# Kernel tuning notes

Measured on AMD Instinct MI355X. Metric: run time of the kernel, lower is better.

## Reference

```python
import jax, jax.numpy as jnp
import numpy as np

B, T, C, H = 4, 4096, 1024, 128

def setup_inputs() -> dict:
    key = jax.random.key(0)
    kx, kk, kq, kv = jax.random.split(key, 4)
    scale = 1.0 / np.sqrt(C)  # mimic Linear init scale
    return {
        'x':  jax.random.normal(kx, (B, T, C), dtype=jnp.float32),
        'Wk': jax.random.normal(kk, (C, H), dtype=jnp.float32) * scale,
        'Wq': jax.random.normal(kq, (C, H), dtype=jnp.float32) * scale,
        'Wv': jax.random.normal(kv, (C, H), dtype=jnp.float32) * scale,
    }

def reference(x, Wk, Wq, Wv):
    # x: [B,T,C]; projections to [B,T,H]
    k = jnp.einsum('btc,ch->bth', x, Wk)
    q = jnp.einsum('btc,ch->bth', x, Wq)
    v = jnp.einsum('btc,ch->bth', x, Wv)
    scale = jnp.asarray(x.shape[-1] and (k.shape[-1] ** -0.5), dtype=x.dtype)
    # scores: [B,T,T]
    scores = jnp.einsum('bqh,bkh->bqk', q, k) * scale
    Tn = x.shape[1]
    causal = jnp.tril(jnp.ones((Tn, Tn), dtype=bool))
    scores = jnp.where(causal[None, :, :], scores, -jnp.inf)
    attn = jax.nn.softmax(scores, axis=-1)
    # dropout=0.0 -> identity
    out = jnp.einsum('bqk,bkh->bqh', attn, v)
    return out
```

## Files before the change

kernel.cpp:

```cpp
#include <hip/hip_runtime.h>
#include <hip/hip_bf16.h>
#include <math.h>

#define B_ 4
#define T_ 4096
#define C_ 1024
#define H_ 128
#define SCALE 0.08838834764831845f
#define SCL2  0.12752934464f

typedef __attribute__((ext_vector_type(8))) short bf16x8;
typedef __attribute__((ext_vector_type(4))) float f32x4;

__device__ __forceinline__ unsigned short f2bf(float f) {
    union { float f; unsigned u; } x; x.f = f;
    unsigned r = x.u + 0x7FFF + ((x.u >> 16) & 1);
    return (unsigned short)(r >> 16);
}
__device__ __forceinline__ float bf2f(unsigned short u) {
    union { unsigned u; float f; } x; x.u = ((unsigned)u) << 16;
    return x.f;
}
__device__ __forceinline__ unsigned cvt_pk_bf16(float a, float b) {
    unsigned r;
    asm("v_cvt_pk_bf16_f32 %0, %1, %2" : "=v"(r) : "v"(a), "v"(b));
    return r;
}
__device__ __forceinline__ float vexp2(float x) {
    float r;
    asm("v_exp_f32 %0, %1" : "=v"(r) : "v"(x));
    return r;
}
__device__ __forceinline__ void cvt16(const float4& a, const float4& b,
                                      const float4& c, const float4& d,
                                      unsigned* t) {
    t[0]=cvt_pk_bf16(a.x,a.y); t[1]=cvt_pk_bf16(a.z,a.w);
    t[2]=cvt_pk_bf16(b.x,b.y); t[3]=cvt_pk_bf16(b.z,b.w);
    t[4]=cvt_pk_bf16(c.x,c.y); t[5]=cvt_pk_bf16(c.z,c.w);
    t[6]=cvt_pk_bf16(d.x,d.y); t[7]=cvt_pk_bf16(d.z,d.w);
}

#define GLOAD16(gsrc, ldst)                                                        \
    __builtin_amdgcn_global_load_lds(                                              \
        (const __attribute__((address_space(1))) unsigned int*)(gsrc),             \
        (__attribute__((address_space(3))) unsigned int*)(ldst), 16, 0, 0)

__global__ __launch_bounds__(256) void wtrans_kernel(
        const float* __restrict__ Wk, const float* __restrict__ Wq,
        const float* __restrict__ Wv, unsigned short* __restrict__ Wt) {
    int tid = blockIdx.x * 256 + threadIdx.x;
    int t = tid >> 17;
    int r = tid & 131071;
    int c = r >> 7;
    int h = r & 127;
    const float* W = (t == 0) ? Wk : (t == 1) ? Wq : Wv;
    Wt[t * 131072 + h * 1024 + c] = f2bf(W[r]);
}

__global__ __launch_bounds__(256, 2) void qkv_gemm6(
        const float* __restrict__ x, const unsigned short* __restrict__ Wt,
        unsigned short* __restrict__ qkv, unsigned short* __restrict__ vT) {
    __shared__ unsigned short As[2][64][72];
    __shared__ unsigned short Bs[2][192][64];

    const int n = blockIdx.x;
    const int mm = n & 255;
    const int nh = n >> 8;
    const int m0 = ((mm & 7) * 32 + (mm >> 3)) * 64;

    const int tid = threadIdx.x;
    const int lane = tid & 63;
    const int w = tid >> 6;
    const int fr = lane & 15;
    const int fq = lane >> 4;

    const int xrow = tid >> 2, xco = (tid & 3) * 16;
    const float* xsrc = x + (long)(m0 + xrow) * C_ + xco;
    const int brl = lane >> 3;
    const int bcolb = (((lane & 7) ^ brl) << 4);
    unsigned short* const bs_flat = &Bs[0][0][0];
    const unsigned short* wbase = Wt + (long)(nh * 192) * 1024;

    f32x4 acc[3][4];
#pragma unroll
    for (int i = 0; i < 3; i++)
#pragma unroll
        for (int rf = 0; rf < 4; rf++) acc[i][rf] = f32x4{0.f, 0.f, 0.f, 0.f};

    float4 xa0, xa1, xa2, xa3, xb0, xb1, xb2, xb3;
    xa0 = ((const float4*)xsrc)[0]; xa1 = ((const float4*)xsrc)[1];
    xa2 = ((const float4*)xsrc)[2]; xa3 = ((const float4*)xsrc)[3];
#pragma unroll
    for (int i = 0; i < 6; i++)
        GLOAD16(wbase + (long)(48*w + 8*i + brl) * 1024 + (bcolb >> 1),
                bs_flat + (w*6 + i) * 512);
    {
        unsigned tw[8];
        cvt16(xa0, xa1, xa2, xa3, tw);
        *(uint4*)&As[0][xrow][xco]     = uint4{tw[0], tw[1], tw[2], tw[3]};
        *(uint4*)&As[0][xrow][xco + 8] = uint4{tw[4], tw[5], tw[6], tw[7]};
    }
    {
        const float* xs = xsrc + 64;
        xa0 = ((const float4*)xs)[0]; xa1 = ((const float4*)xs)[1];
        xa2 = ((const float4*)xs)[2]; xa3 = ((const float4*)xs)[3];
    }

    int cur = 0;
    for (int k = 0; k < 16; ++k) {
        __syncthreads();
        const bool more  = (k + 1) < 16;
        const bool more2 = (k + 2) < 16;
        if (more) {
            if (more2) {
                const float* xs = xsrc + (k + 2) * 64;
                xb0 = ((const float4*)xs)[0]; xb1 = ((const float4*)xs)[1];
                xb2 = ((const float4*)xs)[2]; xb3 = ((const float4*)xs)[3];
            }
            const int boff = (cur ^ 1) * 12288;
#pragma unroll
            for (int i = 0; i < 6; i++)
                GLOAD16(wbase + (long)(48*w + 8*i + brl) * 1024 + (k + 1) * 64 + (bcolb >> 1),
                        bs_flat + boff + (w*6 + i) * 512);
            if (more2) asm volatile("s_waitcnt vmcnt(10)" ::: "memory");
            else       asm volatile("s_waitcnt vmcnt(6)" ::: "memory");
        } else {
            asm volatile("s_waitcnt vmcnt(0)" ::: "memory");
        }
        __syncthreads();

        const char* bsb = (const char*)bs_flat + cur * 24576;
        __builtin_amdgcn_s_setprio(1);
#pragma unroll
        for (int kk = 0; kk < 2; kk++) {
            bf16x8 a[4], bb[3];
#pragma unroll
            for (int rf = 0; rf < 4; rf++)
                a[rf] = *(const bf16x8*)&As[cur][rf*16 + fr][kk*32 + fq*8];
#pragma unroll
            for (int i = 0; i < 3; i++) {
                int row = (w*3 + i) * 16 + fr;
                bb[i] = *(const bf16x8*)(bsb + row*128 + ((((kk<<2) + fq) ^ (fr & 7)) << 4));
            }
#pragma unroll
            for (int i = 0; i < 3; i++)
#pragma unroll
                for (int rf = 0; rf < 4; rf++)
                    acc[i][rf] = __builtin_amdgcn_mfma_f32_16x16x32_bf16(
                        a[rf], bb[i], acc[i][rf], 0, 0, 0);
        }
        __builtin_amdgcn_s_setprio(0);

        if (more) {
            unsigned tw[8];
            cvt16(xa0, xa1, xa2, xa3, tw);
            *(uint4*)&As[cur ^ 1][xrow][xco]     = uint4{tw[0], tw[1], tw[2], tw[3]};
            *(uint4*)&As[cur ^ 1][xrow][xco + 8] = uint4{tw[4], tw[5], tw[6], tw[7]};
            xa0 = xb0; xa1 = xb1; xa2 = xb2; xa3 = xb3;
        }
        cur ^= 1;
    }

#pragma unroll
    for (int i = 0; i < 3; i++) {
        int nfg = nh*12 + w*3 + i;
        int t = nfg >> 3;
        int col = (nfg & 7) * 16 + fr;
        if (t < 2) {
#pragma unroll
            for (int rf = 0; rf < 4; rf++)
#pragma unroll
                for (int r = 0; r < 4; r++) {
                    int row = m0 + rf*16 + fq*4 + r;
                    qkv[(long)t * 2097152 + (long)row * 128 + col] = f2bf(acc[i][rf][r]);
                }
        } else {
            const int bb_ = m0 >> 12;
            const int trow = m0 & 4095;
#pragma unroll
            for (int rf = 0; rf < 4; rf++) {
                uint2 uu;
                uu.x = cvt_pk_bf16(acc[i][rf][0], acc[i][rf][1]);
                uu.y = cvt_pk_bf16(acc[i][rf][2], acc[i][rf][3]);
                *(uint2*)(vT + ((long)(bb_*128 + col)) * 4096 + trow + rf*16 + fq*4) = uu;
            }
        }
    }
}

__global__ __launch_bounds__(512, 4) void flash9_kernel(
        const unsigned short* __restrict__ qkv,
        const unsigned short* __restrict__ vT,
        unsigned short* __restrict__ po0, unsigned short* __restrict__ po1,
        unsigned short* __restrict__ po2, unsigned short* __restrict__ po3,
        float* __restrict__ pm, float* __restrict__ pl) {
    __shared__ unsigned short k_lds[2][64][128];
    __shared__ unsigned short v_lds[2][128][64];

    const int n = blockIdx.x;
    const int half = n >> 8;
    const int m = n & 255;
    const int b = (m & 7) >> 1;
    const int r = ((m >> 3) << 1) | (m & 1);
    const int jj = r & 31;
    const int pq = r >> 5;
    const int qt = half ? (31 - jj) : jj;
    const int p = half * 2 + pq;
    const int q0 = qt * 128;
    const int ntt = (qt + 1) * 2;
    const int t0 = (p * ntt) >> 2;
    const int t1 = ((p + 1) * ntt) >> 2;

    const int tid = threadIdx.x;
    const int w = tid >> 6;
    const int lane = tid & 63;
    const int fr = lane & 15;
    const int fq = lane >> 4;

    const unsigned short* kbase = qkv + (long)b * T_ * H_;
    const unsigned short* vbase = vT + (long)b * H_ * T_;

    const int kcolb0 = ((lane & 15) << 4) ^ ((((lane >> 4)) & 7) << 4);
    const int kcolb1 = ((lane & 15) << 4) ^ (((4 + (lane >> 4)) & 7) << 4);
    const int krl = lane >> 4;
    const int vrl = lane >> 3;
    const int vcolb = ((lane & 7) << 4) ^ (vrl << 4);
    unsigned short* const klds_flat = &k_lds[0][0][0];
    unsigned short* const vlds_flat = &v_lds[0][0][0];
    const int scol = ((fq ^ (fr & 7)) << 4);

    bf16x8 qf[4];
    {
        const unsigned short* qptr = qkv + 2097152 + ((long)b*T_ + q0 + w*16 + fr) * H_;
#pragma unroll
        for (int ks = 0; ks < 4; ks++)
            qf[ks] = *(const bf16x8*)(qptr + ks*32 + fq*8);
    }

    bf16x8 ones;
    {
        union { unsigned short s[8]; bf16x8 v; } oc;
#pragma unroll
        for (int i = 0; i < 8; i++) oc.s[i] = 0x3F80;
        ones = oc.v;
    }

    f32x4 acc[8];
#pragma unroll
    for (int i = 0; i < 8; i++) acc[i] = f32x4{0.f, 0.f, 0.f, 0.f};
    f32x4 acc_l = f32x4{0.f, 0.f, 0.f, 0.f};
    float m_r = -INFINITY;
    const int qrow = q0 + w*16 + fr;

    int cur = 0;
    if (t0 < t1) {
        const int kv0 = t0 * 64;
#pragma unroll
        for (int i = 0; i < 2; i++) {
            int kcolb = i ? kcolb1 : kcolb0;
            GLOAD16(kbase + (long)(kv0 + 8*w + 4*i + krl) * 128 + (kcolb >> 1),
                    klds_flat + w*1024 + i*512);
            GLOAD16(vbase + (long)(16*w + 8*i + vrl) * 4096 + kv0 + (vcolb >> 1),
                    vlds_flat + w*1024 + i*512);
        }
    }

    for (int t = t0; t < t1; ++t) {
        const int kv0 = t * 64;
        asm volatile("s_waitcnt vmcnt(0)" ::: "memory");
        __syncthreads();
        if (t + 1 < t1) {
            const int kv0n = kv0 + 64;
            const int boff = (cur ^ 1) * 8192;
#pragma unroll
            for (int i = 0; i < 2; i++) {
                int kcolb = i ? kcolb1 : kcolb0;
                GLOAD16(kbase + (long)(kv0n + 8*w + 4*i + krl) * 128 + (kcolb >> 1),
                        klds_flat + boff + w*1024 + i*512);
                GLOAD16(vbase + (long)(16*w + 8*i + vrl) * 4096 + kv0n + (vcolb >> 1),
                        vlds_flat + boff + w*1024 + i*512);
            }
        }

        const char* kl = (const char*)k_lds + cur*16384 + fr*256;
        const char* vl = (const char*)v_lds + cur*16384 + fr*128;

        f32x4 s[4];
#pragma unroll
        for (int sf = 0; sf < 4; sf++) s[sf] = f32x4{0.f,0.f,0.f,0.f};
        __builtin_amdgcn_s_setprio(1);
#pragma unroll
        for (int sf = 0; sf < 4; sf++)
#pragma unroll
            for (int ks = 0; ks < 4; ks++) {
                bf16x8 kf = *(const bf16x8*)(kl + sf*4096 + (scol ^ (ks << 6)));
                s[sf] = __builtin_amdgcn_mfma_f32_16x16x32_bf16(kf, qf[ks], s[sf], 0, 0, 0);
            }
        __builtin_amdgcn_s_setprio(0);

        float pmax = -INFINITY;
        if (kv0 + 63 > q0 + 16*w) {
#pragma unroll
            for (int sf = 0; sf < 4; sf++)
#pragma unroll
                for (int rr = 0; rr < 4; rr++) {
                    int kv = kv0 + sf*16 + fq*4 + rr;
                    float sv = s[sf][rr] * SCL2;
                    sv = (kv > qrow) ? -INFINITY : sv;
                    s[sf][rr] = sv;
                    pmax = fmaxf(pmax, sv);
                }
        } else {
#pragma unroll
            for (int sf = 0; sf < 4; sf++)
#pragma unroll
                for (int rr = 0; rr < 4; rr++) {
                    float sv = s[sf][rr] * SCL2;
                    s[sf][rr] = sv;
                    pmax = fmaxf(pmax, sv);
                }
        }

        const bool skip = __all((m_r > -1e37f) & (pmax - m_r <= 11.5f));
        float msub;
        if (skip) {
            msub = m_r;
        } else {
            float mx = fmaxf(pmax, __shfl_xor(pmax, 16, 64));
            mx = fmaxf(mx, __shfl_xor(mx, 32, 64));
            float mn = fmaxf(m_r, mx);
            msub = (mn == -INFINITY) ? 0.f : mn;
            float alpha = vexp2(m_r - msub);
            m_r = mn;
#pragma unroll
            for (int hf = 0; hf < 8; hf++)
#pragma unroll
                for (int rr = 0; rr < 4; rr++) acc[hf][rr] *= alpha;
#pragma unroll
            for (int rr = 0; rr < 4; rr++) acc_l[rr] *= alpha;
        }

        float pv[4][4];
#pragma unroll
        for (int sf = 0; sf < 4; sf++)
#pragma unroll
            for (int rr = 0; rr < 4; rr++)
                pv[sf][rr] = vexp2(s[sf][rr] - msub);

        unsigned pw[8];
#pragma unroll
        for (int sf = 0; sf < 4; sf++) {
            pw[2*sf]   = cvt_pk_bf16(pv[sf][0], pv[sf][1]);
            pw[2*sf+1] = cvt_pk_bf16(pv[sf][2], pv[sf][3]);
        }
        unsigned pbu[2][4];
        pbu[0][0]=0;pbu[0][1]=0;pbu[0][2]=0;pbu[0][3]=0;
        pbu[1][0]=0;pbu[1][1]=0;pbu[1][2]=0;pbu[1][3]=0;
        const int L1 = fr + 16 * ((fq & 1) * 2);
        const int L2 = L1 + 16;
        const int sel = (fq >> 1) & 1;
#pragma unroll
        for (int sf = 0; sf < 4; sf++) {
            unsigned w0 = (unsigned)__shfl((int)pw[2*sf],   L1, 64);
            unsigned w1 = (unsigned)__shfl((int)pw[2*sf+1], L1, 64);
            unsigned w2 = (unsigned)__shfl((int)pw[2*sf],   L2, 64);
            unsigned w3 = (unsigned)__shfl((int)pw[2*sf+1], L2, 64);
            if ((sf & 1) == sel) {
                int k2 = sf >> 1;
                pbu[k2][0] = w0; pbu[k2][1] = w1; pbu[k2][2] = w2; pbu[k2][3] = w3;
            }
        }
        union { unsigned u[4]; bf16x8 v; } pb0c, pb1c;
#pragma unroll
        for (int i = 0; i < 4; i++) { pb0c.u[i] = pbu[0][i]; pb1c.u[i] = pbu[1][i]; }
        bf16x8 pb0 = pb0c.v, pb1 = pb1c.v;

        __builtin_amdgcn_s_setprio(1);
#pragma unroll
        for (int hf = 0; hf < 8; hf++) {
            bf16x8 vf0 = *(const bf16x8*)(vl + hf*2048 + scol);
            bf16x8 vf1 = *(const bf16x8*)(vl + hf*2048 + (scol ^ 64));
            acc[hf] = __builtin_amdgcn_mfma_f32_16x16x32_bf16(vf0, pb0, acc[hf], 0, 0, 0);
            acc[hf] = __builtin_amdgcn_mfma_f32_16x16x32_bf16(vf1, pb1, acc[hf], 0, 0, 0);
        }
        acc_l = __builtin_amdgcn_mfma_f32_16x16x32_bf16(ones, pb0, acc_l, 0, 0, 0);
        acc_l = __builtin_amdgcn_mfma_f32_16x16x32_bf16(ones, pb1, acc_l, 0, 0, 0);
        __builtin_amdgcn_s_setprio(0);
        cur ^= 1;
    }

    unsigned short* po = (p == 0) ? po0 : (p == 1) ? po1 : (p == 2) ? po2 : po3;
    const float l_r = acc_l[0];
    float linv = (l_r > 0.f) ? (1.0f / l_r) : 0.f;
    const long obase = ((long)b * T_ + qrow) * H_;
#pragma unroll
    for (int hf = 0; hf < 8; hf++) {
        uint2 uu;
        uu.x = cvt_pk_bf16(acc[hf][0] * linv, acc[hf][1] * linv);
        uu.y = cvt_pk_bf16(acc[hf][2] * linv, acc[hf][3] * linv);
        *(uint2*)(po + obase + hf*16 + fq*4) = uu;
    }
    if (fq == 0) {
        pm[p * 16384 + b * T_ + qrow] = m_r;
        pl[p * 16384 + b * T_ + qrow] = l_r;
    }
}

__global__ __launch_bounds__(256) void combine4_kernel(
        const unsigned short* __restrict__ po0,
        const unsigned short* __restrict__ po1,
        const unsigned short* __restrict__ po2,
        const unsigned short* __restrict__ po3,
        const float* __restrict__ pm, const float* __restrict__ pl,
        float* __restrict__ out) {
    int idx = blockIdx.x * 256 + threadIdx.x;
    int row = idx >> 4;
    int seg = idx & 15;
    float mv[4], lv[4];
#pragma unroll
    for (int i = 0; i < 4; i++) { mv[i] = pm[i*16384 + row]; lv[i] = pl[i*16384 + row]; }
    float m = fmaxf(fmaxf(mv[0], mv[1]), fmaxf(mv[2], mv[3]));
    float wv[4]; float tot = 0.f;
#pragma unroll
    for (int i = 0; i < 4; i++) {
        wv[i] = (lv[i] > 0.f) ? exp2f(mv[i] - m) * lv[i] : 0.f;
        tot += wv[i];
    }
    float inv = 1.0f / tot;
    long off = (long)row * H_ + seg * 8;
    unsigned short ua[8], ub[8], uc[8], ud[8];
    *(uint4*)ua = *(const uint4*)(po0 + off);
    *(uint4*)ub = *(const uint4*)(po1 + off);
    *(uint4*)uc = *(const uint4*)(po2 + off);
    *(uint4*)ud = *(const uint4*)(po3 + off);
    float* o = out + off;
#pragma unroll
    for (int j2 = 0; j2 < 8; j2++)
        o[j2] = inv * (wv[0] * bf2f(ua[j2]) + wv[1] * bf2f(ub[j2]) +
                       wv[2] * bf2f(uc[j2]) + wv[3] * bf2f(ud[j2]));
}

extern "C" void kernel_launch(void* const* d_in, const int* in_sizes, int n_in,
                              void* d_out, int out_size, void* d_ws, size_t ws_size,
                              hipStream_t stream) {
    (void)in_sizes; (void)n_in; (void)out_size; (void)ws_size;
    const float* x  = (const float*)d_in[0];
    const float* Wk = (const float*)d_in[1];
    const float* Wq = (const float*)d_in[2];
    const float* Wv = (const float*)d_in[3];
    float* out = (float*)d_out;

    unsigned short* Wt  = (unsigned short*)d_ws;
    unsigned short* qkv = Wt + 393216;
    unsigned short* vT  = qkv + 6291456;
    unsigned short* po0 = vT + 2097152;
    unsigned short* po1 = po0 + 2097152;
    unsigned short* po3 = po1 + 2097152;
    unsigned short* po2 = qkv + 4194304;
    float* pm = (float*)d_ws;
    float* pl = pm + 65536;

    wtrans_kernel<<<1536, 256, 0, stream>>>(Wk, Wq, Wv, Wt);
    qkv_gemm6<<<512, 256, 0, stream>>>(x, Wt, qkv, vT);
    flash9_kernel<<<512, 512, 0, stream>>>(qkv, vT, po0, po1, po2, po3, pm, pl);
    combine4_kernel<<<1024, 256, 0, stream>>>(po0, po1, po2, po3, pm, pl, out);
}
```

Measured before the change: 78.60 us.

## Defer PV MFMA of previous tile to overlap with current QK and softmax

The attention loop is software-pipelined: the P·V MFMAs for tile t-1 now run right after the QK^T MFMAs of tile t, before that tile's softmax. The aim is to overlap the softmax VALU and shuffle work with matrix-core work. V is triple-buffered in LDS so the previous tile's V stays valid while the next one is prefetched, and a tail block after the loop drains the last PV step. This raises LDS use per block and keeps P fragments live across iterations, which adds register pressure.

```diff
diff --git a/kernel.cpp b/kernel.cpp
--- a/kernel.cpp
+++ b/kernel.cpp
@@ -188,14 +188,14 @@
     }
 }
 
-__global__ __launch_bounds__(512, 4) void flash9_kernel(
+__global__ __launch_bounds__(512, 4) void flash11_kernel(
         const unsigned short* __restrict__ qkv,
         const unsigned short* __restrict__ vT,
         unsigned short* __restrict__ po0, unsigned short* __restrict__ po1,
         unsigned short* __restrict__ po2, unsigned short* __restrict__ po3,
         float* __restrict__ pm, float* __restrict__ pl) {
     __shared__ unsigned short k_lds[2][64][128];
-    __shared__ unsigned short v_lds[2][128][64];
+    __shared__ unsigned short v_lds[3][128][64];
 
     const int n = blockIdx.x;
     const int half = n >> 8;
@@ -252,7 +252,16 @@
     float m_r = -INFINITY;
     const int qrow = q0 + w*16 + fr;
 
+    bf16x8 pb0, pb1;
+    {
+        union { unsigned u[4]; bf16x8 v; } z;
+        z.u[0]=0; z.u[1]=0; z.u[2]=0; z.u[3]=0;
+        pb0 = z.v; pb1 = z.v;
+    }
+
     int cur = 0;
+    int vsc = t0 % 3;
+    int vsp = 0;
     if (t0 < t1) {
         const int kv0 = t0 * 64;
 #pragma unroll
@@ -261,7 +270,7 @@
             GLOAD16(kbase + (long)(kv0 + 8*w + 4*i + krl) * 128 + (kcolb >> 1),
                     klds_flat + w*1024 + i*512);
             GLOAD16(vbase + (long)(16*w + 8*i + vrl) * 4096 + kv0 + (vcolb >> 1),
-                    vlds_flat + w*1024 + i*512);
+                    vlds_flat + vsc*8192 + w*1024 + i*512);
         }
     }
 
@@ -269,6 +278,7 @@
         const int kv0 = t * 64;
         asm volatile("s_waitcnt vmcnt(0)" ::: "memory");
         __syncthreads();
+        int vsn = vsc + 1; if (vsn == 3) vsn = 0;
         if (t + 1 < t1) {
             const int kv0n = kv0 + 64;
             const int boff = (cur ^ 1) * 8192;
@@ -278,12 +288,11 @@
                 GLOAD16(kbase + (long)(kv0n + 8*w + 4*i + krl) * 128 + (kcolb >> 1),
                         klds_flat + boff + w*1024 + i*512);
                 GLOAD16(vbase + (long)(16*w + 8*i + vrl) * 4096 + kv0n + (vcolb >> 1),
-                        vlds_flat + boff + w*1024 + i*512);
+                        vlds_flat + vsn*8192 + w*1024 + i*512);
             }
         }
 
         const char* kl = (const char*)k_lds + cur*16384 + fr*256;
-        const char* vl = (const char*)v_lds + cur*16384 + fr*128;
 
         f32x4 s[4];
 #pragma unroll
@@ -296,6 +305,18 @@
                 bf16x8 kf = *(const bf16x8*)(kl + sf*4096 + (scol ^ (ks << 6)));
                 s[sf] = __builtin_amdgcn_mfma_f32_16x16x32_bf16(kf, qf[ks], s[sf], 0, 0, 0);
             }
+        if (t > t0) {
+            const char* vlp = (const char*)v_lds + vsp*16384 + fr*128;
+#pragma unroll
+            for (int hf = 0; hf < 8; hf++) {
+                bf16x8 vf0 = *(const bf16x8*)(vlp + hf*2048 + scol);
+                bf16x8 vf1 = *(const bf16x8*)(vlp + hf*2048 + (scol ^ 64));
+                acc[hf] = __builtin_amdgcn_mfma_f32_16x16x32_bf16(vf0, pb0, acc[hf], 0, 0, 0);
+                acc[hf] = __builtin_amdgcn_mfma_f32_16x16x32_bf16(vf1, pb1, acc[hf], 0, 0, 0);
+            }
+            acc_l = __builtin_amdgcn_mfma_f32_16x16x32_bf16(ones, pb0, acc_l, 0, 0, 0);
+            acc_l = __builtin_amdgcn_mfma_f32_16x16x32_bf16(ones, pb1, acc_l, 0, 0, 0);
+        }
         __builtin_amdgcn_s_setprio(0);
 
         float pmax = -INFINITY;
@@ -373,20 +394,22 @@
         union { unsigned u[4]; bf16x8 v; } pb0c, pb1c;
 #pragma unroll
         for (int i = 0; i < 4; i++) { pb0c.u[i] = pbu[0][i]; pb1c.u[i] = pbu[1][i]; }
-        bf16x8 pb0 = pb0c.v, pb1 = pb1c.v;
-
-        __builtin_amdgcn_s_setprio(1);
+        pb0 = pb0c.v; pb1 = pb1c.v;
+
+        vsp = vsc; vsc = vsn; cur ^= 1;
+    }
+
+    if (t1 > t0) {
+        const char* vlp = (const char*)v_lds + vsp*16384 + fr*128;
 #pragma unroll
         for (int hf = 0; hf < 8; hf++) {
-            bf16x8 vf0 = *(const bf16x8*)(vl + hf*2048 + scol);
-            bf16x8 vf1 = *(const bf16x8*)(vl + hf*2048 + (scol ^ 64));
+            bf16x8 vf0 = *(const bf16x8*)(vlp + hf*2048 + scol);
+            bf16x8 vf1 = *(const bf16x8*)(vlp + hf*2048 + (scol ^ 64));
             acc[hf] = __builtin_amdgcn_mfma_f32_16x16x32_bf16(vf0, pb0, acc[hf], 0, 0, 0);
             acc[hf] = __builtin_amdgcn_mfma_f32_16x16x32_bf16(vf1, pb1, acc[hf], 0, 0, 0);
         }
         acc_l = __builtin_amdgcn_mfma_f32_16x16x32_bf16(ones, pb0, acc_l, 0, 0, 0);
         acc_l = __builtin_amdgcn_mfma_f32_16x16x32_bf16(ones, pb1, acc_l, 0, 0, 0);
-        __builtin_amdgcn_s_setprio(0);
-        cur ^= 1;
     }
 
     unsigned short* po = (p == 0) ? po0 : (p == 1) ? po1 : (p == 2) ? po2 : po3;
@@ -462,6 +485,6 @@
 
     wtrans_kernel<<<1536, 256, 0, stream>>>(Wk, Wq, Wv, Wt);
     qkv_gemm6<<<512, 256, 0, stream>>>(x, Wt, qkv, vT);
-    flash9_kernel<<<512, 512, 0, stream>>>(qkv, vT, po0, po1, po2, po3, pm, pl);
+    flash11_kernel<<<512, 512, 0, stream>>>(qkv, vT, po0, po1, po2, po3, pm, pl);
     combine4_kernel<<<1024, 256, 0, stream>>>(po0, po1, po2, po3, pm, pl, out);
 }
```

Measured after the change: 78.65 us. About the same (+0.1%).
